# Optimization experiments

Hardware: AMD Instinct MI355X
Metric: run time of the kernel (lower is better)

Reference implementation:

```python
import jax, jax.numpy as jnp
import numpy as np

B, C, T = 32, 512, 1024
SIG_LO, SIG_HI = 1.0, 10.0   # sigma_range
THR, BETA = 0.5, 0.95        # snn.Leaky(beta=0.95, threshold=thr)
KSIZE = 13


def setup_inputs() -> dict:
    key = jax.random.key(0)
    inp = jax.random.normal(key, (B, 1, C, T), dtype=jnp.float32)
    # nn.Parameter initialized to sigma_range.mean() = 5.5
    w = jnp.float32((SIG_LO + SIG_HI) / 2.0)
    return {"inp": inp, "w": w}


def _gaussian_kernel(sigma):
    # matches gaussian_kernel(size=13): linspace(-6, 6, 13), normalized
    r = jnp.linspace(-(KSIZE // 2), KSIZE // 2, KSIZE).astype(jnp.float32)
    k = jnp.exp(-0.5 * (r / sigma) ** 2)
    return k / k.sum()


def _atan_spike(u):
    # snntorch default ATan surrogate (alpha=2): fwd heaviside, bwd 1/(1+(pi*u)^2)
    soft = jnp.arctan(jnp.pi * u) / jnp.pi
    hard = (u > 0).astype(u.dtype)
    return soft + jax.lax.stop_gradient(hard - soft)


def reference(inp, w):
    x = inp[:, 0]  # (B, C, T)
    # w_eff = sigma_range.mean() + clamp(w, 1, 10); identical for every sample,
    # so the per-sample/per-timestep kernels of the original are all equal.
    sigma = (SIG_LO + SIG_HI) / 2.0 + jnp.clip(w, SIG_LO, SIG_HI)
    k = _gaussian_kernel(sigma)  # (13,)
    # 13-tap Gaussian smoothing along the channel axis, all timesteps at once
    x_mean = jax.lax.conv_general_dilated(
        x[:, None],                    # (B,1,C,T)
        k[None, None, :, None],        # (1,1,13,1)
        window_strides=(1, 1),
        padding=((KSIZE // 2, KSIZE // 2), (0, 0)),
        dimension_numbers=("NCHW", "OIHW", "NCHW"),
    )[:, 0]                            # (B,C,T)
    drive = jnp.transpose(x - x_mean, (2, 0, 1))  # (T,B,C)

    def step(mem, xt):
        # snntorch Leaky, reset_mechanism='subtract'; reset is detached
        reset = jax.lax.stop_gradient((mem > THR).astype(mem.dtype))
        mem = BETA * mem + xt - reset * THR
        spk = _atan_spike(mem - THR)
        return mem, spk

    mem0 = jnp.zeros((B, C), dtype=jnp.float32)
    _, spks = jax.lax.scan(step, mem0, drive)  # (T,B,C)
    return jnp.transpose(spks, (1, 2, 0))[:, None]  # (B,1,C,T)
```

## Files before the change

kernel.cpp:

```cpp
#include <hip/hip_runtime.h>
#include <math.h>

constexpr int Bn = 32;
constexpr int Cn = 512;
constexpr int Tn = 1024;
constexpr int KS = 13;

constexpr int CB   = 32;
constexpr int TT   = 64;
constexpr int NCH  = Tn / TT;
constexpr int DSTR = TT + 1;
constexpr int NCW  = 4;
constexpr int SEG  = CB / NCW;
constexpr int NL   = SEG + KS - 1;


__device__ __forceinline__ void wg_barrier() {
  asm volatile("" ::: "memory");
  __builtin_amdgcn_s_barrier();
  asm volatile("" ::: "memory");
}
__device__ __forceinline__ void lds_fence() {
  asm volatile("s_waitcnt lgkmcnt(0)" ::: "memory");
}

#define SCAN16(DV, TB)                                                   \
  _Pragma("unroll")                                                      \
  for (int j = 0; j < 16; ++j) {                                         \
    const float rthr = (mem > 0.5f) ? 0.5f : 0.0f;   \
    float a_  = __fmul_rn(0.95f, mem);                                   \
    float s2_ = __fadd_rn(a_, DV[j]);                                    \
    mem = __fsub_rn(s2_, rthr);                                          \
    const unsigned int bit = (mem > 0.5f) ? 1u : 0u;                     \
    if ((TB) + j < 32) lo |= bit << ((TB) + j);                          \
    else               hi |= bit << ((TB) + j - 32);                     \
  }

__global__ __launch_bounds__(384, 3)
void snn_fused(const float* __restrict__ x, const float* __restrict__ wp,
               float* __restrict__ out) {
  __shared__ float D[2][CB][DSTR];
  __shared__ unsigned long long Sb[2][CB];

  const int tid = threadIdx.x;
  const int b   = blockIdx.y;
  const int c0  = blockIdx.x * CB;
  const long xbase = (long)b * Cn * Tn;

  float kw[KS];
  {
    float w  = wp[0];
    float wc = fminf(fmaxf(w, 1.0f), 10.0f);
    float sigma = __fadd_rn(5.5f, wc);
    float e[KS];
#pragma unroll
    for (int i = 0; i < KS; ++i) {
      float q = __fdiv_rn((float)(i - 6), sigma);
      float t = __fmul_rn(-0.5f, __fmul_rn(q, q));
      e[i] = (float)exp((double)t);
    }
    float s = __fadd_rn(
        __fadd_rn(__fadd_rn(e[0], e[1]), __fadd_rn(e[2], e[3])),
        __fadd_rn(__fadd_rn(e[4], e[5]), __fadd_rn(e[6], e[7])));
    s = __fadd_rn(s, e[8]);  s = __fadd_rn(s, e[9]);  s = __fadd_rn(s, e[10]);
    s = __fadd_rn(s, e[11]); s = __fadd_rn(s, e[12]);
#pragma unroll
    for (int i = 0; i < KS; ++i) kw[i] = __fdiv_rn(e[i], s);
  }

  if (tid < 64) {
    const int c = tid;
    float mem = 0.0f;
    wg_barrier();
    for (int k = 0; k < NCH; ++k) {
      if (c < CB) {
        const float* Dc = &D[k & 1][c][0];
        unsigned int lo = 0u, hi = 0u;
        float dvA[16], dvB[16];
#pragma unroll
        for (int j = 0; j < 16; ++j) dvA[j] = Dc[j];
#pragma unroll
        for (int j = 0; j < 16; ++j) dvB[j] = Dc[16 + j];
        SCAN16(dvA, 0)
#pragma unroll
        for (int j = 0; j < 16; ++j) dvA[j] = Dc[32 + j];
        SCAN16(dvB, 16)
#pragma unroll
        for (int j = 0; j < 16; ++j) dvB[j] = Dc[48 + j];
        SCAN16(dvA, 32)
        SCAN16(dvB, 48)
        Sb[k & 1][c] = ((unsigned long long)hi << 32) | (unsigned long long)lo;
      }
      lds_fence();
      wg_barrier();
    }
  } else if (tid < 64 + 64 * NCW) {
    const int ctid = tid - 64;
    const int col  = ctid & 63;
    const int segS = (ctid >> 6) * SEG;
    const int cin0 = c0 + segS - 6;

    float xA[NL], xB[NL], xC[NL];

    auto load_chunk = [&](int m, float* dst) {
#pragma unroll
      for (int j = 0; j < NL; ++j) {
        const int gc = cin0 + j;
        float v = 0.0f;
        if (gc >= 0 && gc < Cn)
          v = x[xbase + (long)gc * Tn + m * TT + col];
        dst[j] = v;
      }
    };
    auto conv_chunk = [&](const float* xs, int p) {
#pragma unroll
      for (int r = 0; r < SEG; ++r) {
        float acc = __fmul_rn(kw[0], xs[r]);
#pragma unroll
        for (int i = 1; i < KS; ++i)
          acc = __fadd_rn(acc, __fmul_rn(kw[i], xs[r + i]));
        D[p][segS + r][col] = __fsub_rn(xs[r + 6], acc);
      }
    };

    load_chunk(0, xA);
    load_chunk(1, xB);
    load_chunk(2, xC);
    conv_chunk(xA, 0);
    lds_fence();
    wg_barrier();

#define STEP(K, BL, BC)                                                  \
    do {                                                                 \
      if ((K) + 3 < NCH) load_chunk((K) + 3, BL);                        \
      conv_chunk(BC, ((K) + 1) & 1);                                     \
      lds_fence();                                                       \
      wg_barrier();                                                      \
    } while (0)

    for (int kb = 0; kb < NCH - 1; kb += 3) {
      STEP(kb + 0, xA, xB);
      STEP(kb + 1, xB, xC);
      STEP(kb + 2, xC, xA);
    }
#undef STEP
    wg_barrier();
  } else {
    const int col = tid & 63;
    wg_barrier();
    for (int k = 0; k < NCH; ++k) {
      if (k > 0) {
        const int km  = k - 1;
        const int t0p = km * TT;
#pragma unroll 8
        for (int r = 0; r < CB; ++r) {
          const unsigned long long wb = Sb[km & 1][r];
          const float v = ((wb >> col) & 1ull) ? 1.0f : 0.0f;
          out[xbase + (long)(c0 + r) * Tn + t0p + col] = v;
        }
      }
      wg_barrier();
    }
    {
      const int t0p = (NCH - 1) * TT;
#pragma unroll 8
      for (int r = 0; r < CB; ++r) {
        const unsigned long long wb = Sb[(NCH - 1) & 1][r];
        const float v = ((wb >> col) & 1ull) ? 1.0f : 0.0f;
        out[xbase + (long)(c0 + r) * Tn + t0p + col] = v;
      }
    }
  }
}

extern "C" void kernel_launch(void* const* d_in, const int* in_sizes, int n_in,
                              void* d_out, int out_size, void* d_ws, size_t ws_size,
                              hipStream_t stream) {
  const float* x  = (const float*)d_in[0];
  const float* w  = (const float*)d_in[1];
  float* out      = (float*)d_out;
  dim3 grid(Cn / CB, Bn, 1);
  snn_fused<<<grid, 384, 0, stream>>>(x, w, out);
}
```

Baseline: 127.6 us.

## Stage input tiles via async global-to-LDS loads with halved channel block

The convolution warps now stage input rows directly into triple-buffered LDS tiles using global_load_lds with explicit vmcnt waits, instead of loading into registers. The channel block is halved from 32 to 16 so the grid has more workgroups and occupancy goes up (launch bounds 3 to 6), and the halo rows are shared through LDS. The scan warp reads with float4 LDS loads, and the output warp is restructured to store each chunk right after its barrier. The costs are more redundant halo loading per channel, more LDS per block, and hand-counted vmcnt values that must exactly match the number of loads in flight.

```diff
diff --git a/kernel.cpp b/kernel.cpp
--- a/kernel.cpp
+++ b/kernel.cpp
@@ -6,13 +6,15 @@
 constexpr int Tn = 1024;
 constexpr int KS = 13;
 
-constexpr int CB   = 32;
+constexpr int CB   = 16;
 constexpr int TT   = 64;
 constexpr int NCH  = Tn / TT;
-constexpr int DSTR = TT + 1;
+constexpr int DSTR = 68;
 constexpr int NCW  = 4;
 constexpr int SEG  = CB / NCW;
-constexpr int NL   = SEG + KS - 1;
+constexpr int NW   = SEG + KS - 1;
+constexpr int XR   = CB + KS - 1;
+constexpr int RPW  = XR / NCW;
 
 
 __device__ __forceinline__ void wg_barrier() {
@@ -22,6 +24,14 @@
 }
 __device__ __forceinline__ void lds_fence() {
   asm volatile("s_waitcnt lgkmcnt(0)" ::: "memory");
+}
+#define VMCNT_(n) asm volatile("s_waitcnt vmcnt(" #n ")" ::: "memory")
+#define VMCNT(n) VMCNT_(n)
+
+__device__ __forceinline__ void gload4(const float* g, float* l) {
+  __builtin_amdgcn_global_load_lds(
+      (const __attribute__((address_space(1))) unsigned int*)g,
+      (__attribute__((address_space(3))) unsigned int*)l, 4, 0, 0);
 }
 
 #define SCAN16(DV, TB)                                                   \
@@ -36,60 +46,50 @@
     else               hi |= bit << ((TB) + j - 32);                     \
   }
 
-__global__ __launch_bounds__(384, 3)
+#define LOADG(DV, G)                                                     \
+  { float4 t0_ = Dv[4*(G)+0], t1_ = Dv[4*(G)+1],                         \
+           t2_ = Dv[4*(G)+2], t3_ = Dv[4*(G)+3];                         \
+    DV[0]=t0_.x;  DV[1]=t0_.y;  DV[2]=t0_.z;  DV[3]=t0_.w;               \
+    DV[4]=t1_.x;  DV[5]=t1_.y;  DV[6]=t1_.z;  DV[7]=t1_.w;               \
+    DV[8]=t2_.x;  DV[9]=t2_.y;  DV[10]=t2_.z; DV[11]=t2_.w;              \
+    DV[12]=t3_.x; DV[13]=t3_.y; DV[14]=t3_.z; DV[15]=t3_.w; }
+
+__global__ __launch_bounds__(384, 6)
 void snn_fused(const float* __restrict__ x, const float* __restrict__ wp,
                float* __restrict__ out) {
-  __shared__ float D[2][CB][DSTR];
-  __shared__ unsigned long long Sb[2][CB];
+  __shared__ __align__(16) float XA[XR][TT];
+  __shared__ __align__(16) float XB[XR][TT];
+  __shared__ __align__(16) float XC[XR][TT];
+  __shared__ __align__(16) float DA[CB][DSTR];
+  __shared__ __align__(16) float DB[CB][DSTR];
+  __shared__ unsigned long long SbA[CB], SbB[CB];
 
   const int tid = threadIdx.x;
   const int b   = blockIdx.y;
   const int c0  = blockIdx.x * CB;
   const long xbase = (long)b * Cn * Tn;
 
-  float kw[KS];
-  {
-    float w  = wp[0];
-    float wc = fminf(fmaxf(w, 1.0f), 10.0f);
-    float sigma = __fadd_rn(5.5f, wc);
-    float e[KS];
-#pragma unroll
-    for (int i = 0; i < KS; ++i) {
-      float q = __fdiv_rn((float)(i - 6), sigma);
-      float t = __fmul_rn(-0.5f, __fmul_rn(q, q));
-      e[i] = (float)exp((double)t);
-    }
-    float s = __fadd_rn(
-        __fadd_rn(__fadd_rn(e[0], e[1]), __fadd_rn(e[2], e[3])),
-        __fadd_rn(__fadd_rn(e[4], e[5]), __fadd_rn(e[6], e[7])));
-    s = __fadd_rn(s, e[8]);  s = __fadd_rn(s, e[9]);  s = __fadd_rn(s, e[10]);
-    s = __fadd_rn(s, e[11]); s = __fadd_rn(s, e[12]);
-#pragma unroll
-    for (int i = 0; i < KS; ++i) kw[i] = __fdiv_rn(e[i], s);
-  }
-
   if (tid < 64) {
     const int c = tid;
     float mem = 0.0f;
     wg_barrier();
+    wg_barrier();
     for (int k = 0; k < NCH; ++k) {
       if (c < CB) {
-        const float* Dc = &D[k & 1][c][0];
+        const float4* Dv =
+            (const float4*)((k & 1) ? &DB[c][0] : &DA[c][0]);
         unsigned int lo = 0u, hi = 0u;
         float dvA[16], dvB[16];
-#pragma unroll
-        for (int j = 0; j < 16; ++j) dvA[j] = Dc[j];
-#pragma unroll
-        for (int j = 0; j < 16; ++j) dvB[j] = Dc[16 + j];
+        LOADG(dvA, 0)
+        LOADG(dvB, 1)
         SCAN16(dvA, 0)
-#pragma unroll
-        for (int j = 0; j < 16; ++j) dvA[j] = Dc[32 + j];
+        LOADG(dvA, 2)
         SCAN16(dvB, 16)
-#pragma unroll
-        for (int j = 0; j < 16; ++j) dvB[j] = Dc[48 + j];
+        LOADG(dvB, 3)
         SCAN16(dvA, 32)
         SCAN16(dvB, 48)
-        Sb[k & 1][c] = ((unsigned long long)hi << 32) | (unsigned long long)lo;
+        ((k & 1) ? SbB : SbA)[c] =
+            ((unsigned long long)hi << 32) | (unsigned long long)lo;
       }
       lds_fence();
       wg_barrier();
@@ -97,77 +97,116 @@
   } else if (tid < 64 + 64 * NCW) {
     const int ctid = tid - 64;
     const int col  = ctid & 63;
-    const int segS = (ctid >> 6) * SEG;
-    const int cin0 = c0 + segS - 6;
-
-    float xA[NL], xB[NL], xC[NL];
-
-    auto load_chunk = [&](int m, float* dst) {
-#pragma unroll
-      for (int j = 0; j < NL; ++j) {
-        const int gc = cin0 + j;
-        float v = 0.0f;
-        if (gc >= 0 && gc < Cn)
-          v = x[xbase + (long)gc * Tn + m * TT + col];
-        dst[j] = v;
-      }
+    const int wid  = ctid >> 6;
+    const int segS = wid * SEG;
+    const int rw0  = wid * RPW;
+
+    float kw[KS];
+    {
+      float w  = wp[0];
+      float wc = fminf(fmaxf(w, 1.0f), 10.0f);
+      float sigma = __fadd_rn(5.5f, wc);
+      float e[KS];
+#pragma unroll
+      for (int i = 0; i < KS; ++i) {
+        float q = __fdiv_rn((float)(i - 6), sigma);
+        float t = __fmul_rn(-0.5f, __fmul_rn(q, q));
+        e[i] = (float)exp((double)t);
+      }
+      float s = __fadd_rn(
+          __fadd_rn(__fadd_rn(e[0], e[1]), __fadd_rn(e[2], e[3])),
+          __fadd_rn(__fadd_rn(e[4], e[5]), __fadd_rn(e[6], e[7])));
+      s = __fadd_rn(s, e[8]);  s = __fadd_rn(s, e[9]);  s = __fadd_rn(s, e[10]);
+      s = __fadd_rn(s, e[11]); s = __fadd_rn(s, e[12]);
+#pragma unroll
+      for (int i = 0; i < KS; ++i) kw[i] = __fdiv_rn(e[i], s);
+    }
+
+    long rowoff[RPW];
+#pragma unroll
+    for (int q = 0; q < RPW; ++q) {
+      int gc = c0 - 6 + rw0 + q;
+      gc = gc < 0 ? 0 : (gc >= Cn ? Cn - 1 : gc);
+      rowoff[q] = xbase + (long)gc * Tn;
+    }
+
+    auto stage = [&](int m, float (*X)[TT]) {
+#pragma unroll
+      for (int q = 0; q < RPW; ++q)
+        gload4(x + rowoff[q] + m * TT + col, &X[rw0 + q][0]);
     };
-    auto conv_chunk = [&](const float* xs, int p) {
+
+    const int  cw0  = c0 - 6 + segS;
+    const bool edge = (cw0 < 0) || (cw0 + NW > Cn);
+
+    auto convc = [&](const float (*X)[TT], float (*D)[DSTR]) {
+      float w[NW];
+#pragma unroll
+      for (int i = 0; i < NW; ++i) w[i] = X[segS + i][col];
+      if (edge) {
+#pragma unroll
+        for (int i = 0; i < NW; ++i)
+          if (cw0 + i < 0 || cw0 + i >= Cn) w[i] = 0.0f;
+      }
 #pragma unroll
       for (int r = 0; r < SEG; ++r) {
-        float acc = __fmul_rn(kw[0], xs[r]);
+        float acc = __fmul_rn(kw[0], w[r]);
 #pragma unroll
         for (int i = 1; i < KS; ++i)
-          acc = __fadd_rn(acc, __fmul_rn(kw[i], xs[r + i]));
-        D[p][segS + r][col] = __fsub_rn(xs[r + 6], acc);
+          acc = __fadd_rn(acc, __fmul_rn(kw[i], w[r + i]));
+        D[segS + r][col] = __fsub_rn(w[r + 6], acc);
       }
     };
 
-    load_chunk(0, xA);
-    load_chunk(1, xB);
-    load_chunk(2, xC);
-    conv_chunk(xA, 0);
+    stage(0, XA);
+    stage(1, XB);
+    stage(2, XC);
+    VMCNT(14);
+    wg_barrier();
+    convc(XA, DA);
+    VMCNT(7);
     lds_fence();
     wg_barrier();
 
-#define STEP(K, BL, BC)                                                  \
+#define STEPX(K, XST, XRD, DD, N)                                        \
     do {                                                                 \
-      if ((K) + 3 < NCH) load_chunk((K) + 3, BL);                        \
-      conv_chunk(BC, ((K) + 1) & 1);                                     \
+      if ((K) + 3 < NCH) stage((K) + 3, XST);                            \
+      convc(XRD, DD);                                                    \
+      VMCNT(N);                                                          \
       lds_fence();                                                       \
       wg_barrier();                                                      \
     } while (0)
 
-    for (int kb = 0; kb < NCH - 1; kb += 3) {
-      STEP(kb + 0, xA, xB);
-      STEP(kb + 1, xB, xC);
-      STEP(kb + 2, xC, xA);
-    }
-#undef STEP
+    STEPX(0,  XA, XB, DB, 7);
+    STEPX(1,  XB, XC, DA, 7);
+    STEPX(2,  XC, XA, DB, 7);
+    STEPX(3,  XA, XB, DA, 7);
+    STEPX(4,  XB, XC, DB, 7);
+    STEPX(5,  XC, XA, DA, 7);
+    STEPX(6,  XA, XB, DB, 7);
+    STEPX(7,  XB, XC, DA, 7);
+    STEPX(8,  XC, XA, DB, 7);
+    STEPX(9,  XA, XB, DA, 7);
+    STEPX(10, XB, XC, DB, 7);
+    STEPX(11, XC, XA, DA, 7);
+    STEPX(12, XA, XB, DB, 7);
+    STEPX(13, XB, XC, DA, 0);
+    STEPX(14, XC, XA, DB, 0);
+#undef STEPX
     wg_barrier();
   } else {
     const int col = tid & 63;
     wg_barrier();
+    wg_barrier();
     for (int k = 0; k < NCH; ++k) {
-      if (k > 0) {
-        const int km  = k - 1;
-        const int t0p = km * TT;
-#pragma unroll 8
-        for (int r = 0; r < CB; ++r) {
-          const unsigned long long wb = Sb[km & 1][r];
-          const float v = ((wb >> col) & 1ull) ? 1.0f : 0.0f;
-          out[xbase + (long)(c0 + r) * Tn + t0p + col] = v;
-        }
-      }
       wg_barrier();
-    }
-    {
-      const int t0p = (NCH - 1) * TT;
-#pragma unroll 8
+      const unsigned long long* Sp = (k & 1) ? SbB : SbA;
+      const long obase = xbase + (long)c0 * Tn + (long)k * TT + col;
+#pragma unroll
       for (int r = 0; r < CB; ++r) {
-        const unsigned long long wb = Sb[(NCH - 1) & 1][r];
+        const unsigned long long wb = Sp[r];
         const float v = ((wb >> col) & 1ull) ? 1.0f : 0.0f;
-        out[xbase + (long)(c0 + r) * Tn + t0p + col] = v;
+        out[obase + (long)r * Tn] = v;
       }
     }
   }
```

Measured after the change: 135.9 us. 6.5% more time.

## Double time-chunk width with float2 vector IO and restructured warp-specialized pipeline

Applied to the files above, without the earlier changes.

Raises the time chunk from 64 to 128 so each lane handles two timesteps, using float2 loads from global memory, float2 stores to LDS and float2 stores to the output. This halves the number of barrier-separated pipeline stages. Prefetch depth drops from three buffers to two, and the kernel-weight computation moves into the conv warps only. The writer warps now lag the scan by an extra stage. The scan carries the reset value from the previous spike instead of recomputing the compare. The aim is lower sync and instruction overhead and wider memory transactions, at the cost of less load-latency hiding and more registers per conv thread.

```diff
diff --git a/kernel.cpp b/kernel.cpp
--- a/kernel.cpp
+++ b/kernel.cpp
@@ -7,9 +7,9 @@
 constexpr int KS = 13;
 
 constexpr int CB   = 32;
-constexpr int TT   = 64;
+constexpr int TT   = 128;
 constexpr int NCH  = Tn / TT;
-constexpr int DSTR = TT + 1;
+constexpr int DSTR = TT + 2;
 constexpr int NCW  = 4;
 constexpr int SEG  = CB / NCW;
 constexpr int NL   = SEG + KS - 1;
@@ -24,151 +24,169 @@
   asm volatile("s_waitcnt lgkmcnt(0)" ::: "memory");
 }
 
-#define SCAN16(DV, TB)                                                   \
+#define SSTEP(DV, BP, W)                                                 \
+  {                                                                      \
+    const float rthr = spkf;                                             \
+    float a_  = __fmul_rn(0.95f, mem);                                   \
+    float s2_ = __fadd_rn(a_, (DV));                                     \
+    mem = __fsub_rn(s2_, rthr);                                          \
+    const bool sp_ = (mem > 0.5f);                                       \
+    spkf = sp_ ? 0.5f : 0.0f;                                            \
+    (W) |= sp_ ? (1u << (BP)) : 0u;                                      \
+  }
+
+#define SCAN16(DV2, TB, W)                                               \
   _Pragma("unroll")                                                      \
-  for (int j = 0; j < 16; ++j) {                                         \
-    const float rthr = (mem > 0.5f) ? 0.5f : 0.0f;   \
-    float a_  = __fmul_rn(0.95f, mem);                                   \
-    float s2_ = __fadd_rn(a_, DV[j]);                                    \
-    mem = __fsub_rn(s2_, rthr);                                          \
-    const unsigned int bit = (mem > 0.5f) ? 1u : 0u;                     \
-    if ((TB) + j < 32) lo |= bit << ((TB) + j);                          \
-    else               hi |= bit << ((TB) + j - 32);                     \
+  for (int q = 0; q < 8; ++q) {                                          \
+    SSTEP(DV2[q].x, (((TB) + 2 * q) & 31), W)                            \
+    SSTEP(DV2[q].y, (((TB) + 2 * q + 1) & 31), W)                        \
   }
+
+#define LOADG2(DST, G)                                                   \
+  _Pragma("unroll")                                                      \
+  for (int q = 0; q < 8; ++q) DST[q] = Dv[8 * (G) + q];
 
 __global__ __launch_bounds__(384, 3)
 void snn_fused(const float* __restrict__ x, const float* __restrict__ wp,
                float* __restrict__ out) {
-  __shared__ float D[2][CB][DSTR];
-  __shared__ unsigned long long Sb[2][CB];
+  __shared__ __align__(16) float DA[CB][DSTR];
+  __shared__ __align__(16) float DB[CB][DSTR];
+  __shared__ __align__(16) uint4 SbA[CB];
+  __shared__ __align__(16) uint4 SbB[CB];
 
   const int tid = threadIdx.x;
   const int b   = blockIdx.y;
   const int c0  = blockIdx.x * CB;
   const long xbase = (long)b * Cn * Tn;
 
-  float kw[KS];
-  {
-    float w  = wp[0];
-    float wc = fminf(fmaxf(w, 1.0f), 10.0f);
-    float sigma = __fadd_rn(5.5f, wc);
-    float e[KS];
-#pragma unroll
-    for (int i = 0; i < KS; ++i) {
-      float q = __fdiv_rn((float)(i - 6), sigma);
-      float t = __fmul_rn(-0.5f, __fmul_rn(q, q));
-      e[i] = (float)exp((double)t);
-    }
-    float s = __fadd_rn(
-        __fadd_rn(__fadd_rn(e[0], e[1]), __fadd_rn(e[2], e[3])),
-        __fadd_rn(__fadd_rn(e[4], e[5]), __fadd_rn(e[6], e[7])));
-    s = __fadd_rn(s, e[8]);  s = __fadd_rn(s, e[9]);  s = __fadd_rn(s, e[10]);
-    s = __fadd_rn(s, e[11]); s = __fadd_rn(s, e[12]);
-#pragma unroll
-    for (int i = 0; i < KS; ++i) kw[i] = __fdiv_rn(e[i], s);
-  }
-
   if (tid < 64) {
     const int c = tid;
-    float mem = 0.0f;
+    float mem = 0.0f, spkf = 0.0f;
     wg_barrier();
     for (int k = 0; k < NCH; ++k) {
       if (c < CB) {
-        const float* Dc = &D[k & 1][c][0];
-        unsigned int lo = 0u, hi = 0u;
-        float dvA[16], dvB[16];
-#pragma unroll
-        for (int j = 0; j < 16; ++j) dvA[j] = Dc[j];
-#pragma unroll
-        for (int j = 0; j < 16; ++j) dvB[j] = Dc[16 + j];
-        SCAN16(dvA, 0)
-#pragma unroll
-        for (int j = 0; j < 16; ++j) dvA[j] = Dc[32 + j];
-        SCAN16(dvB, 16)
-#pragma unroll
-        for (int j = 0; j < 16; ++j) dvB[j] = Dc[48 + j];
-        SCAN16(dvA, 32)
-        SCAN16(dvB, 48)
-        Sb[k & 1][c] = ((unsigned long long)hi << 32) | (unsigned long long)lo;
+        const float2* Dv =
+            (const float2*)((k & 1) ? &DB[c][0] : &DA[c][0]);
+        unsigned m0 = 0u, m1 = 0u, m2 = 0u, m3 = 0u;
+        float2 ga[8], gb[8];
+        LOADG2(ga, 0)
+        LOADG2(gb, 1)
+        SCAN16(ga, 0,  m0)  LOADG2(ga, 2)
+        SCAN16(gb, 16, m0)  LOADG2(gb, 3)
+        SCAN16(ga, 32, m1)  LOADG2(ga, 4)
+        SCAN16(gb, 48, m1)  LOADG2(gb, 5)
+        SCAN16(ga, 64, m2)  LOADG2(ga, 6)
+        SCAN16(gb, 80, m2)  LOADG2(gb, 7)
+        SCAN16(ga, 96, m3)
+        SCAN16(gb, 112, m3)
+        ((k & 1) ? SbB : SbA)[c] = make_uint4(m0, m1, m2, m3);
       }
       lds_fence();
       wg_barrier();
     }
+    wg_barrier();
   } else if (tid < 64 + 64 * NCW) {
     const int ctid = tid - 64;
     const int col  = ctid & 63;
     const int segS = (ctid >> 6) * SEG;
     const int cin0 = c0 + segS - 6;
 
-    float xA[NL], xB[NL], xC[NL];
-
-    auto load_chunk = [&](int m, float* dst) {
+    float kw[KS];
+    {
+      float w  = wp[0];
+      float wc = fminf(fmaxf(w, 1.0f), 10.0f);
+      float sigma = __fadd_rn(5.5f, wc);
+      float e[KS];
+#pragma unroll
+      for (int i = 0; i < KS; ++i) {
+        float q = __fdiv_rn((float)(i - 6), sigma);
+        float t = __fmul_rn(-0.5f, __fmul_rn(q, q));
+        e[i] = (float)exp((double)t);
+      }
+      float s = __fadd_rn(
+          __fadd_rn(__fadd_rn(e[0], e[1]), __fadd_rn(e[2], e[3])),
+          __fadd_rn(__fadd_rn(e[4], e[5]), __fadd_rn(e[6], e[7])));
+      s = __fadd_rn(s, e[8]);  s = __fadd_rn(s, e[9]);  s = __fadd_rn(s, e[10]);
+      s = __fadd_rn(s, e[11]); s = __fadd_rn(s, e[12]);
+#pragma unroll
+      for (int i = 0; i < KS; ++i) kw[i] = __fdiv_rn(e[i], s);
+    }
+
+    float2 xA[NL], xB[NL];
+
+    auto load_chunk = [&](int m, float2* dst) {
 #pragma unroll
       for (int j = 0; j < NL; ++j) {
         const int gc = cin0 + j;
-        float v = 0.0f;
+        float2 v = make_float2(0.0f, 0.0f);
         if (gc >= 0 && gc < Cn)
-          v = x[xbase + (long)gc * Tn + m * TT + col];
+          v = *(const float2*)&x[xbase + (long)gc * Tn + m * TT + 2 * col];
         dst[j] = v;
       }
     };
-    auto conv_chunk = [&](const float* xs, int p) {
+    auto conv_chunk = [&](const float2* xs, float (*D)[DSTR]) {
 #pragma unroll
       for (int r = 0; r < SEG; ++r) {
-        float acc = __fmul_rn(kw[0], xs[r]);
-#pragma unroll
-        for (int i = 1; i < KS; ++i)
-          acc = __fadd_rn(acc, __fmul_rn(kw[i], xs[r + i]));
-        D[p][segS + r][col] = __fsub_rn(xs[r + 6], acc);
+        float ax = __fmul_rn(kw[0], xs[r].x);
+        float ay = __fmul_rn(kw[0], xs[r].y);
+#pragma unroll
+        for (int i = 1; i < KS; ++i) {
+          ax = __fadd_rn(ax, __fmul_rn(kw[i], xs[r + i].x));
+          ay = __fadd_rn(ay, __fmul_rn(kw[i], xs[r + i].y));
+        }
+        float2 o = make_float2(__fsub_rn(xs[r + 6].x, ax),
+                               __fsub_rn(xs[r + 6].y, ay));
+        *(float2*)&D[segS + r][2 * col] = o;
       }
     };
 
     load_chunk(0, xA);
     load_chunk(1, xB);
-    load_chunk(2, xC);
-    conv_chunk(xA, 0);
+    conv_chunk(xA, DA);
     lds_fence();
     wg_barrier();
 
-#define STEP(K, BL, BC)                                                  \
+#define STEPC(K, BL, BC, DD)                                             \
     do {                                                                 \
-      if ((K) + 3 < NCH) load_chunk((K) + 3, BL);                        \
-      conv_chunk(BC, ((K) + 1) & 1);                                     \
+      if ((K) + 1 < NCH) load_chunk((K) + 1, BL);                        \
+      conv_chunk(BC, DD);                                                \
       lds_fence();                                                       \
       wg_barrier();                                                      \
     } while (0)
 
-    for (int kb = 0; kb < NCH - 1; kb += 3) {
-      STEP(kb + 0, xA, xB);
-      STEP(kb + 1, xB, xC);
-      STEP(kb + 2, xC, xA);
-    }
-#undef STEP
+    STEPC(1, xA, xB, DB);
+    STEPC(2, xB, xA, DA);
+    STEPC(3, xA, xB, DB);
+    STEPC(4, xB, xA, DA);
+    STEPC(5, xA, xB, DB);
+    STEPC(6, xB, xA, DA);
+    STEPC(7, xA, xB, DB);
+#undef STEPC
+    wg_barrier();
     wg_barrier();
   } else {
     const int col = tid & 63;
+    const bool sel1 = (col & 16) != 0;
+    const bool sel2 = (col & 32) != 0;
+    const unsigned sh = (unsigned)(col & 15) * 2u;
+    wg_barrier();
     wg_barrier();
     for (int k = 0; k < NCH; ++k) {
-      if (k > 0) {
-        const int km  = k - 1;
-        const int t0p = km * TT;
-#pragma unroll 8
-        for (int r = 0; r < CB; ++r) {
-          const unsigned long long wb = Sb[km & 1][r];
-          const float v = ((wb >> col) & 1ull) ? 1.0f : 0.0f;
-          out[xbase + (long)(c0 + r) * Tn + t0p + col] = v;
-        }
+      const uint4* Sp = (k & 1) ? SbB : SbA;
+      const long obase = xbase + (long)c0 * Tn + (long)k * TT + 2 * col;
+#pragma unroll
+      for (int r = 0; r < CB; ++r) {
+        const uint4 q = Sp[r];
+        const unsigned w01 = sel1 ? q.y : q.x;
+        const unsigned w23 = sel1 ? q.w : q.z;
+        const unsigned ws  = sel2 ? w23 : w01;
+        const unsigned bb  = ws >> sh;
+        float2 o;
+        o.x = (bb & 1u) ? 1.0f : 0.0f;
+        o.y = (bb & 2u) ? 1.0f : 0.0f;
+        *(float2*)&out[obase + (long)r * Tn] = o;
       }
       wg_barrier();
-    }
-    {
-      const int t0p = (NCH - 1) * TT;
-#pragma unroll 8
-      for (int r = 0; r < CB; ++r) {
-        const unsigned long long wb = Sb[(NCH - 1) & 1][r];
-        const float v = ((wb >> col) & 1ull) ? 1.0f : 0.0f;
-        out[xbase + (long)(c0 + r) * Tn + t0p + col] = v;
-      }
     }
   }
 }
```

Result: slower. 144.3 us (+13.1%).
